# Optimization experiments

Measured on AMD Instinct MI355X. Metric: run time of the kernel, lower is better.

## Reference

```python
import jax, jax.numpy as jnp
import numpy as np

NUM_HEADS = 8

def setup_inputs() -> dict:
    key = jax.random.key(0)
    ks = jax.random.split(key, 5)
    B, N, C = 8, 16384, 256
    x = jax.random.normal(ks[0], (B, N, C), dtype=jnp.float32)
    Wq = jax.random.normal(ks[1], (C, C), dtype=jnp.float32) * 0.02
    Wkv = jax.random.normal(ks[2], (2 * C, C), dtype=jnp.float32) * 0.02
    Wproj = jax.random.normal(ks[3], (C, C), dtype=jnp.float32) * 0.02
    bproj = jnp.zeros((C,), dtype=jnp.float32)
    return {"x": x, "Wq": Wq, "Wkv": Wkv, "Wproj": Wproj, "bproj": bproj}


def reference(x, Wq, Wkv, Wproj, bproj):
    B, N, C = x.shape
    h = NUM_HEADS
    d = C // h
    # q, kv projections (torch Linear: x @ W.T)
    q = jnp.einsum('bnc,oc->bno', x, Wq).reshape(B, N, h, d).transpose(0, 2, 1, 3)   # [B,h,N,d]
    kv = jnp.einsum('bnc,oc->bno', x, Wkv).reshape(B, N, 2, h, d)
    k = kv[:, :, 0].transpose(0, 2, 1, 3)  # [B,h,N,d]
    v = kv[:, :, 1].transpose(0, 2, 1, 3)  # [B,h,N,d]
    # feature map: elu(x) + 1 (positive)
    q = jax.nn.elu(q) + 1.0
    k = jax.nn.elu(k) + 1.0
    # normalizer: q . sum_n k_n
    k_sum = k.sum(axis=2)                                    # [B,h,d]
    D_inv = 1.0 / jnp.maximum(jnp.einsum('bhnd,bhd->bhn', q, k_sum), 1e-6)  # [B,h,N]
    # linear-attention context: k^T @ v  ->  [B,h,d,d]
    context = jnp.einsum('bhnd,bhne->bhde', k, v)
    attn = jnp.einsum('bhnd,bhde->bhne', q, context) * D_inv[..., None]     # [B,h,N,d]
    out = attn.transpose(0, 2, 1, 3).reshape(B, N, C)
    out = jnp.einsum('bnc,oc->bno', out, Wproj) + bproj
    return out
```

## Files before the change

kernel.cpp:

```cpp
#include <hip/hip_runtime.h>
#include <hip/hip_bf16.h>
#include <cstdint>
#include <cstddef>

typedef __attribute__((ext_vector_type(8))) short short8;
typedef __attribute__((ext_vector_type(4))) float f32x4;

#define DEVI static __device__ __forceinline__

DEVI unsigned short f2bf(float f) {
  unsigned u = __float_as_uint(f);
  unsigned r = u + 0x7fffu + ((u >> 16) & 1u);
  return (unsigned short)(r >> 16);
}
DEVI float bf2f(unsigned short s) {
  return __uint_as_float(((unsigned)s) << 16);
}
DEVI unsigned pack2(float a, float b) {
  return (unsigned)f2bf(a) | ((unsigned)f2bf(b) << 16);
}

DEVI void gload16(const void* g, void* l) {
  __builtin_amdgcn_global_load_lds(
      (__attribute__((address_space(1))) void*)g,
      (__attribute__((address_space(3))) void*)l, 16, 0, 0);
}

__global__ __launch_bounds__(256) void prep_w(
    const float* __restrict__ Wq, const float* __restrict__ Wkv,
    const float* __restrict__ Wp, unsigned short* __restrict__ wcat,
    unsigned short* __restrict__ wpb) {
  int i = blockIdx.x * 256 + threadIdx.x;
  if (i < 196608) {
    float v = (i < 65536) ? Wq[i] : Wkv[i - 65536];
    wcat[i] = f2bf(v);
  } else {
    int j = i - 196608;
    wpb[j] = f2bf(Wp[j]);
  }
}

__global__ __launch_bounds__(256) void qkv_ctx(
    const float* __restrict__ x, const unsigned short* __restrict__ wcat,
    unsigned short* __restrict__ Q, float* __restrict__ pctx,
    float* __restrict__ pksum) {
  const int t = threadIdx.x;
  const int lane = t & 63, w = t >> 6;
  const int p = blockIdx.x;
  const size_t row0 = (size_t)p * 64;
  const int fr = lane & 15, fq = lane >> 4;

  __shared__ __align__(16) unsigned char smem[40960];
  unsigned char* const wb0 = smem;
  unsigned char* const wb1 = smem + 16384;
  unsigned char* const kT = smem + 32768;
  unsigned char* const vT = smem + 36864;

  const short ob = (short)0x3F80;
  const short8 ones = {ob, ob, ob, ob, ob, ob, ob, ob};

  short8 xfc[8];
  {
    const float* xr = x + (row0 + w * 16 + fr) * 256;
#pragma unroll
    for (int ks = 0; ks < 8; ++ks) {
      float4 a = *(const float4*)(xr + ks * 32 + fq * 8);
      float4 b2 = *(const float4*)(xr + ks * 32 + fq * 8 + 4);
      union { unsigned u[4]; short8 s; } cv;
      cv.u[0] = pack2(a.x, a.y);
      cv.u[1] = pack2(a.z, a.w);
      cv.u[2] = pack2(b2.x, b2.y);
      cv.u[3] = pack2(b2.z, b2.w);
      xfc[ks] = cv.s;
    }
  }

  const int segr = lane >> 5;
  const int segc = (lane & 31) * 16;
  auto stage_w = [&](unsigned char* buf, int s) {
    int wr0 = (s < 8) ? s * 32
                      : (((s & 1) == 0) ? 256 + ((s - 8) >> 1) * 32
                                        : 512 + ((s - 8) >> 1) * 32);
#pragma unroll
    for (int i = 0; i < 4; ++i) {
      int seg = w * 4 + i;
      int rloc = seg * 2 + segr;
      gload16((const char*)wcat + (size_t)(wr0 + rloc) * 512 +
                  (segc ^ ((rloc & 7) << 4)),
              buf + seg * 1024);
    }
  };

  auto ctx_head = [&](int h) {
    const int dp = w >> 1, ep = w & 1;
    f32x4 cacc = {0.f, 0.f, 0.f, 0.f};
    f32x4 sacc = {0.f, 0.f, 0.f, 0.f};
    const int rka = dp * 16 + fr;
    const int rkb = ep * 16 + fr;
#pragma unroll
    for (int ks = 0; ks < 2; ++ks) {
      short8 ak = *(const short8*)(kT + rka * 128 +
                                   ((ks * 64 + fq * 16) ^ ((rka & 7) << 4)));
      short8 bv = *(const short8*)(vT + rkb * 128 +
                                   ((ks * 64 + fq * 16) ^ ((rkb & 7) << 4)));
      cacc = __builtin_amdgcn_mfma_f32_16x16x32_bf16(ak, bv, cacc, 0, 0, 0);
      if (ep == 0)
        sacc = __builtin_amdgcn_mfma_f32_16x16x32_bf16(ak, ones, sacc, 0, 0, 0);
    }
    float* pc = pctx + ((size_t)(p * 8 + h)) * 1024;
#pragma unroll
    for (int reg = 0; reg < 4; ++reg) {
      int d = dp * 16 + fq * 4 + reg;
      int e = ep * 16 + fr;
      pc[d * 32 + e] = cacc[reg];
    }
    if (ep == 0 && fr == 0) {
#pragma unroll
      for (int reg = 0; reg < 4; ++reg) {
        int d = dp * 16 + fq * 4 + reg;
        pksum[((size_t)(p * 8 + h)) * 32 + d] = sacc[reg];
      }
    }
  };

  stage_w(wb0, 0);
  __syncthreads();

  unsigned char* const bb = kT + w * 1280;

  for (int s = 0; s < 24; ++s) {
    if (s >= 10 && (s & 1) == 0) ctx_head((s - 10) >> 1);
    if (s < 23) stage_w(((s & 1) == 0) ? wb1 : wb0, s + 1);

    const unsigned char* wbuf = ((s & 1) == 0) ? wb0 : wb1;

    if (s < 8) {
      f32x4 acc[2] = {{0.f, 0.f, 0.f, 0.f}, {0.f, 0.f, 0.f, 0.f}};
#pragma unroll
      for (int ks = 0; ks < 8; ++ks) {
#pragma unroll
        for (int j = 0; j < 2; ++j) {
          int rb = j * 16 + fr;
          short8 wf = *(const short8*)(wbuf + rb * 512 +
                                       ((ks * 64 + fq * 16) ^ ((rb & 7) << 4)));
          acc[j] = __builtin_amdgcn_mfma_f32_16x16x32_bf16(wf, xfc[ks], acc[j],
                                                           0, 0, 0);
        }
      }
#pragma unroll
      for (int j = 0; j < 2; ++j) {
        float v0 = acc[j][0], v1 = acc[j][1], v2 = acc[j][2], v3 = acc[j][3];
        v0 = (v0 > 0.f) ? (v0 + 1.f) : __expf(v0);
        v1 = (v1 > 0.f) ? (v1 + 1.f) : __expf(v1);
        v2 = (v2 > 0.f) ? (v2 + 1.f) : __expf(v2);
        v3 = (v3 > 0.f) ? (v3 + 1.f) : __expf(v3);
        uint2 pk;
        pk.x = pack2(v0, v1);
        pk.y = pack2(v2, v3);
        *(uint2*)(bb + fr * 80 + j * 32 + fq * 8) = pk;
      }
      {
        int rowq = lane >> 2, c4 = lane & 3;
        uint4 u = *(const uint4*)(bb + rowq * 80 + c4 * 16);
        *(uint4*)((char*)Q + (row0 + w * 16 + rowq) * 512 + s * 64 + c4 * 16) = u;
      }
    } else {
      f32x4 acc[2] = {{0.f, 0.f, 0.f, 0.f}, {0.f, 0.f, 0.f, 0.f}};
#pragma unroll
      for (int ks = 0; ks < 8; ++ks) {
#pragma unroll
        for (int j = 0; j < 2; ++j) {
          int rb = j * 16 + fr;
          short8 wf = *(const short8*)(wbuf + rb * 512 +
                                       ((ks * 64 + fq * 16) ^ ((rb & 7) << 4)));
          acc[j] = __builtin_amdgcn_mfma_f32_16x16x32_bf16(xfc[ks], wf, acc[j],
                                                           0, 0, 0);
        }
      }
      __syncthreads();

      const bool isK = ((s & 1) == 0);
      unsigned char* dstT = isK ? kT : vT;
#pragma unroll
      for (int j = 0; j < 2; ++j) {
        int d = j * 16 + fr;
        float v0 = acc[j][0], v1 = acc[j][1], v2 = acc[j][2], v3 = acc[j][3];
        if (isK) {
          v0 = (v0 > 0.f) ? (v0 + 1.f) : __expf(v0);
          v1 = (v1 > 0.f) ? (v1 + 1.f) : __expf(v1);
          v2 = (v2 > 0.f) ? (v2 + 1.f) : __expf(v2);
          v3 = (v3 > 0.f) ? (v3 + 1.f) : __expf(v3);
        }
        uint2 pk;
        pk.x = pack2(v0, v1);
        pk.y = pack2(v2, v3);
        *(uint2*)(dstT + d * 128 + ((w * 32 + fq * 8) ^ ((d & 7) << 4))) = pk;
      }
    }
    __syncthreads();
  }
  ctx_head(7);
}

__global__ __launch_bounds__(256) void ctx_final2(
    const float* __restrict__ pctx, const float* __restrict__ pksum,
    unsigned short* __restrict__ ctxT, float* __restrict__ ksum) {
  int bh = blockIdx.x;
  int b = bh >> 3, h = bh & 7;
  int t = threadIdx.x;
  int d = t >> 3, e4 = (t & 7) * 4;
  float s[4] = {0.f, 0.f, 0.f, 0.f};
  for (int pp = 0; pp < 256; ++pp) {
    const float* q = pctx + ((size_t)((b * 256 + pp) * 8 + h)) * 1024 + d * 32 + e4;
    s[0] += q[0]; s[1] += q[1]; s[2] += q[2]; s[3] += q[3];
  }
  unsigned short* cc = ctxT + (size_t)bh * 2048;
#pragma unroll
  for (int e2 = 0; e2 < 4; ++e2) {
    int e = e4 + e2;
    unsigned short hi = f2bf(s[e2]);
    float lo = s[e2] - bf2f(hi);
    cc[e * 32 + d] = hi;
    cc[1024 + e * 32 + d] = f2bf(lo);
  }
  __shared__ float ksp[8][32];
  int d2 = t & 31, ch = t >> 5;
  float ss = 0.f;
  for (int pp = ch; pp < 256; pp += 8)
    ss += pksum[((size_t)((b * 256 + pp) * 8 + h)) * 32 + d2];
  ksp[ch][d2] = ss;
  __syncthreads();
  if (t < 32) {
    float r = 0.f;
#pragma unroll
    for (int c = 0; c < 8; ++c) r += ksp[c][t];
    ksum[bh * 32 + t] = r;
  }
}

__global__ __launch_bounds__(512) void attn_proj(
    const unsigned short* __restrict__ Q,
    const unsigned short* __restrict__ ctxT,
    const float* __restrict__ ksum,
    const unsigned short* __restrict__ wpb,
    const float* __restrict__ bias,
    float* __restrict__ out) {
  const int t = threadIdx.x;
  const int lane = t & 63, w = t >> 6;
  const int panel = blockIdx.x;
  const int b = panel >> 8;
  const size_t row0 = (size_t)panel * 64;
  const int fr = lane & 15, fq = lane >> 4;

  __shared__ __align__(16) unsigned char qa[32768];
  __shared__ __align__(16) unsigned char wpS[2][16384];
  __shared__ float ksumL[256];
  __shared__ float Dinv_s[64][8];

#pragma unroll
  for (int s = 0; s < 4; ++s) {
    int seg = w * 4 + s;
    int row = seg * 2 + (lane >> 5);
    gload16((const char*)Q + (row0 + row) * 512 +
                (((lane & 31) * 16) ^ ((row & 7) << 4)),
            qa + seg * 1024);
  }
  if (w == 0) gload16((const char*)(ksum + b * 256) + lane * 16, (void*)ksumL);
  __syncthreads();

  {
    int r = t >> 3, h = t & 7;
    const unsigned char* qrow = qa + r * 512;
    int swzr = (r & 7) << 4;
    float s = 0.f;
#pragma unroll
    for (int dd = 0; dd < 16; ++dd) {
      unsigned u = *(const unsigned*)(qrow + ((h * 64 + dd * 4) ^ swzr));
      s += __uint_as_float(u << 16) * ksumL[h * 32 + dd * 2] +
           __uint_as_float(u & 0xffff0000u) * ksumL[h * 32 + dd * 2 + 1];
    }
    Dinv_s[r][h] = 1.f / fmaxf(s, 1e-6f);
  }

  const int rg = w >> 2, hg = w & 3;
  f32x4 sacc[2][2][2];
#pragma unroll
  for (int h2 = 0; h2 < 2; ++h2)
#pragma unroll
    for (int i = 0; i < 2; ++i)
#pragma unroll
      for (int j = 0; j < 2; ++j)
#pragma unroll
        for (int c = 0; c < 4; ++c) sacc[h2][i][j][c] = 0.f;

#pragma unroll
  for (int h2 = 0; h2 < 2; ++h2) {
    int h = hg * 2 + h2;
    const char* cbh = (const char*)ctxT + ((size_t)(b * 8 + h)) * 4096;
    short8 bhi[2], blo[2];
#pragma unroll
    for (int j = 0; j < 2; ++j) {
      int e = j * 16 + fr;
      bhi[j] = *(const short8*)(cbh + e * 64 + fq * 16);
      blo[j] = *(const short8*)(cbh + 2048 + e * 64 + fq * 16);
    }
#pragma unroll
    for (int i = 0; i < 2; ++i) {
      int ra = rg * 32 + i * 16 + fr;
      short8 af = *(const short8*)(qa + ra * 512 +
                                   ((h * 64 + fq * 16) ^ ((ra & 7) << 4)));
#pragma unroll
      for (int j = 0; j < 2; ++j) {
        sacc[h2][i][j] = __builtin_amdgcn_mfma_f32_16x16x32_bf16(
            af, bhi[j], sacc[h2][i][j], 0, 0, 0);
        sacc[h2][i][j] = __builtin_amdgcn_mfma_f32_16x16x32_bf16(
            af, blo[j], sacc[h2][i][j], 0, 0, 0);
      }
    }
  }
  __syncthreads();

#pragma unroll
  for (int h2 = 0; h2 < 2; ++h2) {
    int h = hg * 2 + h2;
#pragma unroll
    for (int i = 0; i < 2; ++i)
#pragma unroll
      for (int j = 0; j < 2; ++j)
#pragma unroll
        for (int reg = 0; reg < 4; ++reg) {
          int r = rg * 32 + i * 16 + fq * 4 + reg;
          int e = j * 16 + fr;
          float v = sacc[h2][i][j][reg] * Dinv_s[r][h];
          *(unsigned short*)(qa + r * 512 +
                             ((h * 64 + e * 2) ^ ((r & 7) << 4))) = f2bf(v);
        }
  }

  auto stage_wp = [&](int q, unsigned char* buf) {
#pragma unroll
    for (int i = 0; i < 2; ++i) {
      int seg = w * 2 + i;
      int rloc = seg * 2 + (lane >> 5);
      gload16((const char*)wpb + (size_t)(q * 32 + rloc) * 512 +
                  (((lane & 31) * 16) ^ ((rloc & 7) << 4)),
              buf + seg * 1024);
    }
  };
  stage_wp(0, wpS[0]);
  __syncthreads();

  const int rw = w >> 1, cw = w & 1;
  const int ra2 = rw * 16 + fr;
  const int sra2 = (ra2 & 7) << 4;
  for (int q = 0; q < 8; ++q) {
    if (q < 7) stage_wp(q + 1, wpS[(q + 1) & 1]);
    const unsigned char* wbuf = wpS[q & 1];
    f32x4 oacc = {0.f, 0.f, 0.f, 0.f};
#pragma unroll
    for (int ks = 0; ks < 8; ++ks) {
      short8 af = *(const short8*)(qa + ra2 * 512 + ((ks * 64 + fq * 16) ^ sra2));
      int rb = cw * 16 + fr;
      short8 wf = *(const short8*)(wbuf + rb * 512 +
                                   ((ks * 64 + fq * 16) ^ ((rb & 7) << 4)));
      oacc = __builtin_amdgcn_mfma_f32_16x16x32_bf16(af, wf, oacc, 0, 0, 0);
    }
    float bj = bias[q * 32 + cw * 16 + fr];
    float* orow = out + row0 * 256 + (size_t)(rw * 16 + fq * 4) * 256 +
                  q * 32 + cw * 16 + fr;
#pragma unroll
    for (int reg = 0; reg < 4; ++reg) orow[reg * 256] = oacc[reg] + bj;
    __syncthreads();
  }
}

extern "C" void kernel_launch(void* const* d_in, const int* in_sizes, int n_in,
                              void* d_out, int out_size, void* d_ws, size_t ws_size,
                              hipStream_t stream) {
  const float* x = (const float*)d_in[0];
  const float* Wq = (const float*)d_in[1];
  const float* Wkv = (const float*)d_in[2];
  const float* Wproj = (const float*)d_in[3];
  const float* bproj = (const float*)d_in[4];
  float* out = (float*)d_out;

  char* ws = (char*)d_ws;
  unsigned short* Q = (unsigned short*)(ws);
  unsigned short* wcat = (unsigned short*)(ws + 67108864);
  unsigned short* wpb = (unsigned short*)(ws + 67502080);
  float* pctx = (float*)(ws + 67633152);
  float* pksum = (float*)(ws + 134742016);
  unsigned short* ctxT = (unsigned short*)(ws + 136839168);
  float* ksum = (float*)(ws + 137101312);

  prep_w<<<1024, 256, 0, stream>>>(Wq, Wkv, Wproj, wcat, wpb);
  qkv_ctx<<<2048, 256, 0, stream>>>(x, wcat, Q, pctx, pksum);
  ctx_final2<<<64, 256, 0, stream>>>(pctx, pksum, ctxT, ksum);
  attn_proj<<<2048, 512, 0, stream>>>(Q, ctxT, ksum, wpb, bproj, out);
}
```

Measured before the change: 197.5 us.

## Double qkv_ctx tile to 128 rows with 512 threads, halving partial context outputs

The qkv_ctx kernel now processes 128 rows per block with 8 waves in a 4x2 layout. Each wave reuses one weight fragment across two row sub-tiles, and the K/V staging is rescheduled so each head's context is computed while the next head's projection runs. Partial context and k-sum buffers shrink by half, which cuts global writes and the reduction work in ctx_final2. The trade is higher register use from two x fragment sets, 48KB of LDS, and only half the waves doing the context MFMAs.

```diff
diff --git a/kernel.cpp b/kernel.cpp
--- a/kernel.cpp
+++ b/kernel.cpp
@@ -40,28 +40,30 @@
   }
 }
 
-__global__ __launch_bounds__(256) void qkv_ctx(
+__global__ __launch_bounds__(512, 4) void qkv_ctx(
     const float* __restrict__ x, const unsigned short* __restrict__ wcat,
     unsigned short* __restrict__ Q, float* __restrict__ pctx,
     float* __restrict__ pksum) {
   const int t = threadIdx.x;
   const int lane = t & 63, w = t >> 6;
-  const int p = blockIdx.x;
-  const size_t row0 = (size_t)p * 64;
+  const int wr = w >> 1, wc = w & 1;
+  const int blk = blockIdx.x;
+  const size_t row0 = (size_t)blk * 128;
   const int fr = lane & 15, fq = lane >> 4;
 
-  __shared__ __align__(16) unsigned char smem[40960];
+  __shared__ __align__(16) unsigned char smem[49152];
   unsigned char* const wb0 = smem;
   unsigned char* const wb1 = smem + 16384;
   unsigned char* const kT = smem + 32768;
-  unsigned char* const vT = smem + 36864;
+  unsigned char* const vT = smem + 40960;
 
   const short ob = (short)0x3F80;
   const short8 ones = {ob, ob, ob, ob, ob, ob, ob, ob};
 
-  short8 xfc[8];
-  {
-    const float* xr = x + (row0 + w * 16 + fr) * 256;
+  short8 xfc[2][8];
+#pragma unroll
+  for (int i = 0; i < 2; ++i) {
+    const float* xr = x + (row0 + wr * 32 + i * 16 + fr) * 256;
 #pragma unroll
     for (int ks = 0; ks < 8; ++ks) {
       float4 a = *(const float4*)(xr + ks * 32 + fq * 8);
@@ -71,7 +73,7 @@
       cv.u[1] = pack2(a.z, a.w);
       cv.u[2] = pack2(b2.x, b2.y);
       cv.u[3] = pack2(b2.z, b2.w);
-      xfc[ks] = cv.s;
+      xfc[i][ks] = cv.s;
     }
   }
 
@@ -82,8 +84,8 @@
                       : (((s & 1) == 0) ? 256 + ((s - 8) >> 1) * 32
                                         : 512 + ((s - 8) >> 1) * 32);
 #pragma unroll
-    for (int i = 0; i < 4; ++i) {
-      int seg = w * 4 + i;
+    for (int i = 0; i < 2; ++i) {
+      int seg = w * 2 + i;
       int rloc = seg * 2 + segr;
       gload16((const char*)wcat + (size_t)(wr0 + rloc) * 512 +
                   (segc ^ ((rloc & 7) << 4)),
@@ -92,33 +94,35 @@
   };
 
   auto ctx_head = [&](int h) {
-    const int dp = w >> 1, ep = w & 1;
-    f32x4 cacc = {0.f, 0.f, 0.f, 0.f};
-    f32x4 sacc = {0.f, 0.f, 0.f, 0.f};
-    const int rka = dp * 16 + fr;
-    const int rkb = ep * 16 + fr;
-#pragma unroll
-    for (int ks = 0; ks < 2; ++ks) {
-      short8 ak = *(const short8*)(kT + rka * 128 +
-                                   ((ks * 64 + fq * 16) ^ ((rka & 7) << 4)));
-      short8 bv = *(const short8*)(vT + rkb * 128 +
-                                   ((ks * 64 + fq * 16) ^ ((rkb & 7) << 4)));
-      cacc = __builtin_amdgcn_mfma_f32_16x16x32_bf16(ak, bv, cacc, 0, 0, 0);
-      if (ep == 0)
-        sacc = __builtin_amdgcn_mfma_f32_16x16x32_bf16(ak, ones, sacc, 0, 0, 0);
-    }
-    float* pc = pctx + ((size_t)(p * 8 + h)) * 1024;
-#pragma unroll
-    for (int reg = 0; reg < 4; ++reg) {
-      int d = dp * 16 + fq * 4 + reg;
-      int e = ep * 16 + fr;
-      pc[d * 32 + e] = cacc[reg];
-    }
-    if (ep == 0 && fr == 0) {
+    if (w < 4) {
+      const int dp = w >> 1, ep = w & 1;
+      f32x4 cacc = {0.f, 0.f, 0.f, 0.f};
+      f32x4 sacc = {0.f, 0.f, 0.f, 0.f};
+      const int rka = dp * 16 + fr;
+      const int rkb = ep * 16 + fr;
+#pragma unroll
+      for (int ks = 0; ks < 4; ++ks) {
+        short8 ak = *(const short8*)(kT + rka * 256 +
+                                     ((ks * 64 + fq * 16) ^ ((rka & 7) << 4)));
+        short8 bv = *(const short8*)(vT + rkb * 256 +
+                                     ((ks * 64 + fq * 16) ^ ((rkb & 7) << 4)));
+        cacc = __builtin_amdgcn_mfma_f32_16x16x32_bf16(ak, bv, cacc, 0, 0, 0);
+        if (ep == 0)
+          sacc = __builtin_amdgcn_mfma_f32_16x16x32_bf16(ak, ones, sacc, 0, 0, 0);
+      }
+      float* pc = pctx + ((size_t)(blk * 8 + h)) * 1024;
 #pragma unroll
       for (int reg = 0; reg < 4; ++reg) {
         int d = dp * 16 + fq * 4 + reg;
-        pksum[((size_t)(p * 8 + h)) * 32 + d] = sacc[reg];
+        int e = ep * 16 + fr;
+        pc[d * 32 + e] = cacc[reg];
+      }
+      if (ep == 0 && fr == 0) {
+#pragma unroll
+        for (int reg = 0; reg < 4; ++reg) {
+          int d = dp * 16 + fq * 4 + reg;
+          pksum[((size_t)(blk * 8 + h)) * 32 + d] = sacc[reg];
+        }
       }
     }
   };
@@ -128,74 +132,94 @@
 
   unsigned char* const bb = kT + w * 1280;
 
-  for (int s = 0; s < 24; ++s) {
-    if (s >= 10 && (s & 1) == 0) ctx_head((s - 10) >> 1);
-    if (s < 23) stage_w(((s & 1) == 0) ? wb1 : wb0, s + 1);
-
-    const unsigned char* wbuf = ((s & 1) == 0) ? wb0 : wb1;
-
-    if (s < 8) {
-      f32x4 acc[2] = {{0.f, 0.f, 0.f, 0.f}, {0.f, 0.f, 0.f, 0.f}};
+#pragma unroll
+  for (int s = 0; s < 8; ++s) {
+    stage_w((s & 1) ? wb0 : wb1, s + 1);
+    const unsigned char* wbuf = (s & 1) ? wb1 : wb0;
+
+    f32x4 acc[2] = {{0.f, 0.f, 0.f, 0.f}, {0.f, 0.f, 0.f, 0.f}};
+    const int rb = wc * 16 + fr;
+    const int swb = (rb & 7) << 4;
+#pragma unroll
+    for (int ks = 0; ks < 8; ++ks) {
+      short8 wf = *(const short8*)(wbuf + rb * 512 + ((ks * 64 + fq * 16) ^ swb));
+      acc[0] = __builtin_amdgcn_mfma_f32_16x16x32_bf16(wf, xfc[0][ks], acc[0], 0, 0, 0);
+      acc[1] = __builtin_amdgcn_mfma_f32_16x16x32_bf16(wf, xfc[1][ks], acc[1], 0, 0, 0);
+    }
+#pragma unroll
+    for (int i = 0; i < 2; ++i) {
+      float v0 = acc[i][0], v1 = acc[i][1], v2 = acc[i][2], v3 = acc[i][3];
+      v0 = (v0 > 0.f) ? (v0 + 1.f) : __expf(v0);
+      v1 = (v1 > 0.f) ? (v1 + 1.f) : __expf(v1);
+      v2 = (v2 > 0.f) ? (v2 + 1.f) : __expf(v2);
+      v3 = (v3 > 0.f) ? (v3 + 1.f) : __expf(v3);
+      uint2 pk;
+      pk.x = pack2(v0, v1);
+      pk.y = pack2(v2, v3);
+      *(uint2*)(bb + (i * 16 + fr) * 40 + fq * 8) = pk;
+    }
+    {
+      int rowq = lane >> 1, ch = lane & 1;
+      uint4 u = *(const uint4*)(bb + rowq * 40 + ch * 16);
+      *(uint4*)((char*)Q + (row0 + wr * 32 + rowq) * 512 + s * 64 + wc * 32 +
+                ch * 16) = u;
+    }
+    __syncthreads();
+  }
+
+#pragma unroll
+  for (int h = 0; h < 8; ++h) {
+    const int sk = 8 + 2 * h;
+    stage_w(wb1, sk + 1);
+    f32x4 kacc[2] = {{0.f, 0.f, 0.f, 0.f}, {0.f, 0.f, 0.f, 0.f}};
+    {
+      const int rb = wc * 16 + fr;
+      const int swb = (rb & 7) << 4;
 #pragma unroll
       for (int ks = 0; ks < 8; ++ks) {
-#pragma unroll
-        for (int j = 0; j < 2; ++j) {
-          int rb = j * 16 + fr;
-          short8 wf = *(const short8*)(wbuf + rb * 512 +
-                                       ((ks * 64 + fq * 16) ^ ((rb & 7) << 4)));
-          acc[j] = __builtin_amdgcn_mfma_f32_16x16x32_bf16(wf, xfc[ks], acc[j],
-                                                           0, 0, 0);
-        }
-      }
-#pragma unroll
-      for (int j = 0; j < 2; ++j) {
-        float v0 = acc[j][0], v1 = acc[j][1], v2 = acc[j][2], v3 = acc[j][3];
-        v0 = (v0 > 0.f) ? (v0 + 1.f) : __expf(v0);
-        v1 = (v1 > 0.f) ? (v1 + 1.f) : __expf(v1);
-        v2 = (v2 > 0.f) ? (v2 + 1.f) : __expf(v2);
-        v3 = (v3 > 0.f) ? (v3 + 1.f) : __expf(v3);
-        uint2 pk;
-        pk.x = pack2(v0, v1);
-        pk.y = pack2(v2, v3);
-        *(uint2*)(bb + fr * 80 + j * 32 + fq * 8) = pk;
-      }
-      {
-        int rowq = lane >> 2, c4 = lane & 3;
-        uint4 u = *(const uint4*)(bb + rowq * 80 + c4 * 16);
-        *(uint4*)((char*)Q + (row0 + w * 16 + rowq) * 512 + s * 64 + c4 * 16) = u;
-      }
-    } else {
-      f32x4 acc[2] = {{0.f, 0.f, 0.f, 0.f}, {0.f, 0.f, 0.f, 0.f}};
+        short8 wf = *(const short8*)(wb0 + rb * 512 + ((ks * 64 + fq * 16) ^ swb));
+        kacc[0] = __builtin_amdgcn_mfma_f32_16x16x32_bf16(xfc[0][ks], wf, kacc[0], 0, 0, 0);
+        kacc[1] = __builtin_amdgcn_mfma_f32_16x16x32_bf16(xfc[1][ks], wf, kacc[1], 0, 0, 0);
+      }
+    }
+    if (h > 0) ctx_head(h - 1);
+    __syncthreads();
+
+#pragma unroll
+    for (int i = 0; i < 2; ++i) {
+      int d = wc * 16 + fr;
+      float v0 = kacc[i][0], v1 = kacc[i][1], v2 = kacc[i][2], v3 = kacc[i][3];
+      v0 = (v0 > 0.f) ? (v0 + 1.f) : __expf(v0);
+      v1 = (v1 > 0.f) ? (v1 + 1.f) : __expf(v1);
+      v2 = (v2 > 0.f) ? (v2 + 1.f) : __expf(v2);
+      v3 = (v3 > 0.f) ? (v3 + 1.f) : __expf(v3);
+      uint2 pk;
+      pk.x = pack2(v0, v1);
+      pk.y = pack2(v2, v3);
+      int nb = wr * 64 + i * 32 + fq * 8;
+      *(uint2*)(kT + d * 256 + (nb ^ ((d & 7) << 4))) = pk;
+    }
+
+    if (h < 7) stage_w(wb0, sk + 2);
+    f32x4 vacc[2] = {{0.f, 0.f, 0.f, 0.f}, {0.f, 0.f, 0.f, 0.f}};
+    {
+      const int rb = wc * 16 + fr;
+      const int swb = (rb & 7) << 4;
 #pragma unroll
       for (int ks = 0; ks < 8; ++ks) {
-#pragma unroll
-        for (int j = 0; j < 2; ++j) {
-          int rb = j * 16 + fr;
-          short8 wf = *(const short8*)(wbuf + rb * 512 +
-                                       ((ks * 64 + fq * 16) ^ ((rb & 7) << 4)));
-          acc[j] = __builtin_amdgcn_mfma_f32_16x16x32_bf16(xfc[ks], wf, acc[j],
-                                                           0, 0, 0);
-        }
-      }
-      __syncthreads();
-
-      const bool isK = ((s & 1) == 0);
-      unsigned char* dstT = isK ? kT : vT;
-#pragma unroll
-      for (int j = 0; j < 2; ++j) {
-        int d = j * 16 + fr;
-        float v0 = acc[j][0], v1 = acc[j][1], v2 = acc[j][2], v3 = acc[j][3];
-        if (isK) {
-          v0 = (v0 > 0.f) ? (v0 + 1.f) : __expf(v0);
-          v1 = (v1 > 0.f) ? (v1 + 1.f) : __expf(v1);
-          v2 = (v2 > 0.f) ? (v2 + 1.f) : __expf(v2);
-          v3 = (v3 > 0.f) ? (v3 + 1.f) : __expf(v3);
-        }
-        uint2 pk;
-        pk.x = pack2(v0, v1);
-        pk.y = pack2(v2, v3);
-        *(uint2*)(dstT + d * 128 + ((w * 32 + fq * 8) ^ ((d & 7) << 4))) = pk;
-      }
+        short8 wf = *(const short8*)(wb1 + rb * 512 + ((ks * 64 + fq * 16) ^ swb));
+        vacc[0] = __builtin_amdgcn_mfma_f32_16x16x32_bf16(xfc[0][ks], wf, vacc[0], 0, 0, 0);
+        vacc[1] = __builtin_amdgcn_mfma_f32_16x16x32_bf16(xfc[1][ks], wf, vacc[1], 0, 0, 0);
+      }
+    }
+#pragma unroll
+    for (int i = 0; i < 2; ++i) {
+      int e = wc * 16 + fr;
+      uint2 pk;
+      pk.x = pack2(vacc[i][0], vacc[i][1]);
+      pk.y = pack2(vacc[i][2], vacc[i][3]);
+      int nb = wr * 64 + i * 32 + fq * 8;
+      *(uint2*)(vT + e * 256 + (nb ^ ((e & 7) << 4))) = pk;
     }
     __syncthreads();
   }
@@ -210,8 +234,8 @@
   int t = threadIdx.x;
   int d = t >> 3, e4 = (t & 7) * 4;
   float s[4] = {0.f, 0.f, 0.f, 0.f};
-  for (int pp = 0; pp < 256; ++pp) {
-    const float* q = pctx + ((size_t)((b * 256 + pp) * 8 + h)) * 1024 + d * 32 + e4;
+  for (int pp = 0; pp < 128; ++pp) {
+    const float* q = pctx + ((size_t)((b * 128 + pp) * 8 + h)) * 1024 + d * 32 + e4;
     s[0] += q[0]; s[1] += q[1]; s[2] += q[2]; s[3] += q[3];
   }
   unsigned short* cc = ctxT + (size_t)bh * 2048;
@@ -226,8 +250,8 @@
   __shared__ float ksp[8][32];
   int d2 = t & 31, ch = t >> 5;
   float ss = 0.f;
-  for (int pp = ch; pp < 256; pp += 8)
-    ss += pksum[((size_t)((b * 256 + pp) * 8 + h)) * 32 + d2];
+  for (int pp = ch; pp < 128; pp += 8)
+    ss += pksum[((size_t)((b * 128 + pp) * 8 + h)) * 32 + d2];
   ksp[ch][d2] = ss;
   __syncthreads();
   if (t < 32) {
@@ -389,12 +413,12 @@
   unsigned short* wcat = (unsigned short*)(ws + 67108864);
   unsigned short* wpb = (unsigned short*)(ws + 67502080);
   float* pctx = (float*)(ws + 67633152);
-  float* pksum = (float*)(ws + 134742016);
-  unsigned short* ctxT = (unsigned short*)(ws + 136839168);
-  float* ksum = (float*)(ws + 137101312);
+  float* pksum = (float*)(ws + 101187584);
+  unsigned short* ctxT = (unsigned short*)(ws + 102236160);
+  float* ksum = (float*)(ws + 102498304);
 
   prep_w<<<1024, 256, 0, stream>>>(Wq, Wkv, Wproj, wcat, wpb);
-  qkv_ctx<<<2048, 256, 0, stream>>>(x, wcat, Q, pctx, pksum);
+  qkv_ctx<<<1024, 512, 0, stream>>>(x, wcat, Q, pctx, pksum);
   ctx_final2<<<64, 256, 0, stream>>>(pctx, pksum, ctxT, ksum);
   attn_proj<<<2048, 512, 0, stream>>>(Q, ctxT, ksum, wpb, bproj, out);
 }
```

New measurement: 177.0 us. 1.12x faster.
